# Kernel tuning notes

Measured on AMD Instinct MI355X. Metric: run time of the kernel, lower is better.

Reference implementation:

```python
import jax, jax.numpy as jnp
import numpy as np

N_POINTS = 131072  # 32 clouds * 4096 points
N_SEG = 32


def setup_inputs() -> dict:
    key = jax.random.key(0)
    ks = jax.random.split(key, 8)
    x = jax.random.normal(ks[0], (N_POINTS, 256), dtype=jnp.float32)
    pos = jax.random.normal(ks[1], (N_POINTS, 3), dtype=jnp.float32)
    # sorted segment ids, every segment non-empty (equal-size clouds)
    batch = jnp.repeat(jnp.arange(N_SEG, dtype=jnp.int32), N_POINTS // N_SEG)
    def lin(k, fan_in, fan_out):
        s = 1.0 / np.sqrt(fan_in)
        return jax.random.uniform(k, (fan_in, fan_out), jnp.float32, -s, s)
    W1 = lin(ks[2], 259, 256); b1 = jnp.zeros((256,), jnp.float32)
    W2 = lin(ks[3], 256, 512); b2 = jnp.zeros((512,), jnp.float32)
    W3 = lin(ks[4], 512, 1024); b3 = jnp.zeros((1024,), jnp.float32)
    return {"x": x, "pos": pos, "batch": batch,
            "W1": W1, "b1": b1, "W2": W2, "b2": b2, "W3": W3, "b3": b3}


def reference(x, pos, batch, W1, b1, W2, b2, W3, b3):
    # concat point features with coordinates: [N, 256+3]
    h = jnp.concatenate([x, pos], axis=1)
    # shared point-wise MLP (Linear + ReLU per layer)
    h = jax.nn.relu(h @ W1 + b1)   # [N, 256]
    h = jax.nn.relu(h @ W2 + b2)   # [N, 512]
    h = jax.nn.relu(h @ W3 + b3)   # [N, 1024]
    # global_max_pool: batch-indexed segment max -> [N_SEG, 1024]
    return jax.ops.segment_max(h, batch, num_segments=N_SEG)
```

## Files before the change

### kernel.cpp

```cpp
#include <hip/hip_runtime.h>
#include <stdint.h>

typedef unsigned short ushort_t;
typedef short shortx8 __attribute__((ext_vector_type(8)));
typedef float floatx4 __attribute__((ext_vector_type(4)));
typedef unsigned short ushortx8 __attribute__((ext_vector_type(8)));

__device__ __forceinline__ unsigned short f2bf(float f) {
  union { float f; unsigned int u; } v; v.f = f;
  unsigned int u = v.u;
  return (unsigned short)((u + 0x7fffu + ((u >> 16) & 1u)) >> 16);
}

__device__ __forceinline__ void gload_lds16(const void* g, void* l) {
  __builtin_amdgcn_global_load_lds(
      (const __attribute__((address_space(1))) unsigned int*)g,
      (__attribute__((address_space(3))) unsigned int*)l, 16, 0, 0);
}

__global__ void prep_w_k(const float* __restrict__ W1, const float* __restrict__ W2,
                         const float* __restrict__ W3, ushort_t* __restrict__ W1T,
                         ushort_t* __restrict__ W2T, ushort_t* __restrict__ W3T) {
  int idx = blockIdx.x * blockDim.x + threadIdx.x;
  const float* in; ushort_t* out; int K, N;
  if (idx < 256 * 256)                  { in = W1; out = W1T; K = 256; N = 256; }
  else if (idx < 256 * 256 + 512 * 256) { idx -= 256 * 256; in = W2; out = W2T; K = 256; N = 512; }
  else if (idx < 256 * 256 + 512 * 256 + 1024 * 512) {
    idx -= 256 * 256 + 512 * 256; in = W3; out = W3T; K = 512; N = 1024;
  } else return;
  int n = idx / K, k = idx - n * K;
  out[idx] = f2bf(in[k * N + n]);
}

template <int K, int NOUT, int MODE>
__global__ __launch_bounds__(256, 2) void gemm_kernel(
    const ushort_t* __restrict__ A, const ushort_t* __restrict__ BT,
    const float* __restrict__ bias, ushort_t* __restrict__ C,
    const float* __restrict__ pos, const float* __restrict__ W1tail,
    float* __restrict__ pool, const float* __restrict__ Afp) {
  __shared__ __align__(16) ushort_t As[128 * 64];
  __shared__ __align__(16) ushort_t Bs[128 * 64];

  constexpr int GY = NOUT / 128;
  const int wlin = blockIdx.x + blockIdx.y * gridDim.x;
  const int nwg = gridDim.x * GY;
  const int swz = (wlin & 7) * (nwg >> 3) + (wlin >> 3);
  const int m0 = (swz / GY) * 128;
  const int n0 = (swz % GY) * 128;
  const int tid = threadIdx.x;
  const int w = tid >> 6;
  const int l = tid & 63;
  const int wm = w >> 1, wn = w & 1;
  const int lane16 = l & 15, lq = l >> 4;
  const int s7 = lane16 & 7;

  const int srow = l >> 3;
  const int sg = (l & 7) ^ srow;

  floatx4 acc[4][4] = {};

  for (int k0 = 0; k0 < K; k0 += 64) {
    if (MODE == 1) {
#pragma unroll
      for (int rep = 0; rep < 4; ++rep) {
        const int g = rep * 256 + tid;
        const int row = g >> 3, slot = g & 7;
        const int sgr = slot ^ (row & 7);
        const float4* src = (const float4*)(Afp + (size_t)(m0 + row) * K + k0 + sgr * 8);
        float4 a = src[0], b = src[1];
        ushortx8 v;
        v[0] = f2bf(a.x); v[1] = f2bf(a.y); v[2] = f2bf(a.z); v[3] = f2bf(a.w);
        v[4] = f2bf(b.x); v[5] = f2bf(b.y); v[6] = f2bf(b.z); v[7] = f2bf(b.w);
        *(ushortx8*)(As + row * 64 + slot * 8) = v;
      }
    } else {
#pragma unroll
      for (int r = 0; r < 4; ++r) {
        const int c = r * 4 + w;
        const int row = c * 8 + srow;
        gload_lds16(A + (size_t)(m0 + row) * K + k0 + sg * 8, As + c * 512);
      }
    }
#pragma unroll
    for (int r = 0; r < 4; ++r) {
      const int c = r * 4 + w;
      const int row = c * 8 + srow;
      gload_lds16(BT + (size_t)(n0 + row) * K + k0 + sg * 8, Bs + c * 512);
    }
    __syncthreads();
#pragma unroll
    for (int kk = 0; kk < 2; ++kk) {
      shortx8 af[4], bfr[4];
#pragma unroll
      for (int i = 0; i < 4; ++i) {
        const int row = wm * 64 + i * 16 + lane16;
        af[i] = *(const shortx8*)(As + row * 64 + ((kk * 4 + lq) ^ s7) * 8);
      }
#pragma unroll
      for (int j = 0; j < 4; ++j) {
        const int row = wn * 64 + j * 16 + lane16;
        bfr[j] = *(const shortx8*)(Bs + row * 64 + ((kk * 4 + lq) ^ s7) * 8);
      }
#pragma unroll
      for (int i = 0; i < 4; ++i)
#pragma unroll
        for (int j = 0; j < 4; ++j)
          acc[i][j] = __builtin_amdgcn_mfma_f32_16x16x32_bf16(af[i], bfr[j], acc[i][j], 0, 0, 0);
    }
    __syncthreads();
  }

  float bv[4];
#pragma unroll
  for (int j = 0; j < 4; ++j) bv[j] = bias[n0 + wn * 64 + j * 16 + lane16];

#pragma unroll
  for (int i = 0; i < 4; ++i) {
#pragma unroll
    for (int r = 0; r < 4; ++r) {
      int m = m0 + wm * 64 + i * 16 + lq * 4 + r;
      float p0 = 0.f, p1 = 0.f, p2 = 0.f;
      if (MODE == 1) { p0 = pos[m * 3 + 0]; p1 = pos[m * 3 + 1]; p2 = pos[m * 3 + 2]; }
#pragma unroll
      for (int j = 0; j < 4; ++j) {
        int n = n0 + wn * 64 + j * 16 + lane16;
        float v = acc[i][j][r] + bv[j];
        if (MODE == 1) v += p0 * W1tail[n] + p1 * W1tail[256 + n] + p2 * W1tail[512 + n];
        v = fmaxf(v, 0.0f);
        C[(size_t)m * NOUT + n] = f2bf(v);
      }
    }
  }
}

template <int K, int NOUT, int MODE>
__global__ __launch_bounds__(512, 2) void gemm256_kernel(
    const ushort_t* __restrict__ A, const ushort_t* __restrict__ BT,
    const float* __restrict__ bias, ushort_t* __restrict__ C,
    float* __restrict__ pool) {
  __shared__ __align__(16) ushort_t As[2][256 * 64];
  __shared__ __align__(16) ushort_t Bs[2][256 * 64];

  constexpr int GY = NOUT / 256;
  constexpr int T = K / 64;

  const int wlin = blockIdx.x + blockIdx.y * gridDim.x;
  const int nwg = gridDim.x * GY;
  const int swz = (wlin & 7) * (nwg >> 3) + (wlin >> 3);
  const int m0 = (swz / GY) * 256;
  const int n0 = (swz % GY) * 256;

  const int tid = threadIdx.x;
  const int w8 = tid >> 6;
  const int l = tid & 63;
  const int wm = w8 >> 2, wn = w8 & 3;
  const int lane16 = l & 15, lq = l >> 4;
  const int s7 = lane16 & 7;

  const int sgl = (l & 7) ^ (l >> 3);
  const int lrow = l >> 3;
  const int arow0 = w8 << 3;
  const int brow0 = ((w8 >> 1) << 6) + ((w8 & 1) << 3);

  floatx4 acc[2][4][4] = {};
  shortx8 af[4][2];
  shortx8 bfr[4][2];

#define STAGEA(bb, tt, h, rb)                                                  \
  do {                                                                         \
    const int base_ = (h)*64 + (rb)*128 + arow0;                               \
    gload_lds16(A + (size_t)(m0 + base_ + lrow) * K + (tt)*64 + sgl * 8,       \
                &As[bb][base_ * 64]);                                          \
  } while (0)
#define STAGEB(bb, tt, h, rb)                                                  \
  do {                                                                         \
    const int base_ = brow0 + (h)*32 + (rb)*16;                                \
    gload_lds16(BT + (size_t)(n0 + base_ + lrow) * K + (tt)*64 + sgl * 8,      \
                &Bs[bb][base_ * 64]);                                          \
  } while (0)
#define STAGE_ALL(bb, tt)                                                      \
  do {                                                                         \
    STAGEA(bb, tt, 0, 0); STAGEA(bb, tt, 0, 1);                                \
    STAGEB(bb, tt, 0, 0); STAGEB(bb, tt, 0, 1);                                \
    STAGEB(bb, tt, 1, 0); STAGEB(bb, tt, 1, 1);                                \
    STAGEA(bb, tt, 1, 0); STAGEA(bb, tt, 1, 1);                                \
  } while (0)
#define READA(bb, mh)                                                          \
  {                                                                            \
    _Pragma("unroll") for (int i = 0; i < 4; ++i) {                            \
      const int row_ = wm * 128 + (mh)*64 + i * 16 + lane16;                   \
      _Pragma("unroll") for (int ks = 0; ks < 2; ++ks) {                       \
        const int sl_ = ((ks << 2) | lq) ^ s7;                                 \
        af[i][ks] = *(const shortx8*)(&As[bb][row_ * 64 + sl_ * 8]);           \
      }                                                                        \
    }                                                                          \
  }
#define READB(bb, jh)                                                          \
  {                                                                            \
    _Pragma("unroll") for (int jj = 0; jj < 2; ++jj) {                         \
      const int j_ = (jh)*2 + jj;                                              \
      const int row_ = wn * 64 + j_ * 16 + lane16;                             \
      _Pragma("unroll") for (int ks = 0; ks < 2; ++ks) {                       \
        const int sl_ = ((ks << 2) | lq) ^ s7;                                 \
        bfr[j_][ks] = *(const shortx8*)(&Bs[bb][row_ * 64 + sl_ * 8]);         \
      }                                                                        \
    }                                                                          \
  }
#define DOMFMA(mh, jh)                                                         \
  {                                                                            \
    _Pragma("unroll") for (int ks = 0; ks < 2; ++ks)                           \
    _Pragma("unroll") for (int i = 0; i < 4; ++i)                              \
    _Pragma("unroll") for (int jj = 0; jj < 2; ++jj)                           \
      acc[mh][i][(jh)*2 + jj] = __builtin_amdgcn_mfma_f32_16x16x32_bf16(       \
          af[i][ks], bfr[(jh)*2 + jj][ks], acc[mh][i][(jh)*2 + jj], 0, 0, 0);  \
  }
#define WAITV(n)                                                               \
  do {                                                                         \
    asm volatile("s_waitcnt vmcnt(" #n ")" ::: "memory");                      \
    __builtin_amdgcn_sched_barrier(0);                                         \
  } while (0)
#define BAR()                                                                  \
  do {                                                                         \
    __builtin_amdgcn_sched_barrier(0);                                         \
    asm volatile("" ::: "memory");                                             \
    __builtin_amdgcn_s_barrier();                                              \
    asm volatile("" ::: "memory");                                             \
    __builtin_amdgcn_sched_barrier(0);                                         \
  } while (0)

  STAGE_ALL(0, 0);

  for (int t = 0; t < T; ++t) {
    const int buf = t & 1;
    WAITV(0);
    BAR();
    if (t + 1 < T) STAGE_ALL(buf ^ 1, t + 1);
    READA(buf, 0);
    READB(buf, 0);
    READB(buf, 1);
    __builtin_amdgcn_s_setprio(1);
    DOMFMA(0, 0);
    DOMFMA(0, 1);
    __builtin_amdgcn_s_setprio(0);
    __builtin_amdgcn_sched_barrier(0);
    READA(buf, 1);
    __builtin_amdgcn_s_setprio(1);
    DOMFMA(1, 0);
    DOMFMA(1, 1);
    __builtin_amdgcn_s_setprio(0);
  }
#undef STAGEA
#undef STAGEB
#undef STAGE_ALL
#undef READA
#undef READB
#undef DOMFMA
#undef WAITV
#undef BAR

  float bv[4];
#pragma unroll
  for (int j = 0; j < 4; ++j) bv[j] = bias[n0 + wn * 64 + j * 16 + lane16];

  if (MODE == 2) {
    const int seg = m0 >> 12;
#pragma unroll
    for (int j = 0; j < 4; ++j) {
      float vmax = 0.0f;
#pragma unroll
      for (int mh = 0; mh < 2; ++mh)
#pragma unroll
        for (int i = 0; i < 4; ++i)
#pragma unroll
          for (int r = 0; r < 4; ++r) vmax = fmaxf(vmax, acc[mh][i][j][r] + bv[j]);
      vmax = fmaxf(vmax, 0.0f);
      vmax = fmaxf(vmax, __shfl_xor(vmax, 16, 64));
      vmax = fmaxf(vmax, __shfl_xor(vmax, 32, 64));
      if (l < 16) {
        const int n = n0 + wn * 64 + j * 16 + lane16;
        atomicMax((int*)(pool + (size_t)seg * NOUT + n), __float_as_int(vmax));
      }
    }
  } else {
#pragma unroll
    for (int mh = 0; mh < 2; ++mh)
#pragma unroll
      for (int i = 0; i < 4; ++i)
#pragma unroll
        for (int r = 0; r < 4; ++r) {
          const int m = m0 + wm * 128 + mh * 64 + i * 16 + lq * 4 + r;
#pragma unroll
          for (int j = 0; j < 4; ++j) {
            const int n = n0 + wn * 64 + j * 16 + lane16;
            C[(size_t)m * NOUT + n] = f2bf(fmaxf(acc[mh][i][j][r] + bv[j], 0.0f));
          }
        }
  }
}


extern "C" void kernel_launch(void* const* d_in, const int* in_sizes, int n_in,
                              void* d_out, int out_size, void* d_ws, size_t ws_size,
                              hipStream_t stream) {
  const float* x   = (const float*)d_in[0];
  const float* pos = (const float*)d_in[1];
  const float* W1 = (const float*)d_in[3];
  const float* b1 = (const float*)d_in[4];
  const float* W2 = (const float*)d_in[5];
  const float* b2 = (const float*)d_in[6];
  const float* W3 = (const float*)d_in[7];
  const float* b3 = (const float*)d_in[8];
  float* out = (float*)d_out;

  const int M = in_sizes[0] / 256;

  char* ws = (char*)d_ws;
  ushort_t* H2  = (ushort_t*)ws;
  ushort_t* H1  = (ushort_t*)(ws + (size_t)M * 512 * 2);
  ushort_t* W1T = (ushort_t*)(ws + (size_t)M * 512 * 2 + (size_t)M * 256 * 2);
  ushort_t* W2T = W1T + 256 * 256;
  ushort_t* W3T = W2T + 512 * 256;

  const int ntr = 256 * 256 + 512 * 256 + 1024 * 512;
  prep_w_k<<<(ntr + 255) / 256, 256, 0, stream>>>(W1, W2, W3, W1T, W2T, W3T);

  gemm_kernel<256, 256, 1><<<dim3(M / 128, 2), 256, 0, stream>>>(
      nullptr, W1T, b1, H1, pos, W1 + 256 * 256, nullptr, x);
  gemm256_kernel<256, 512, 0><<<dim3(M / 256, 2), 512, 0, stream>>>(
      H1, W2T, b2, H2, nullptr);
  gemm256_kernel<512, 1024, 2><<<dim3(M / 256, 4), 512, 0, stream>>>(
      H2, W3T, b3, nullptr, out);
}
```

Before: 416.3 us.

## Interleave GEMM global->LDS staging with MFMA phases using fine-grained waits

Splits the per-tile global-to-LDS prefetch into four groups and issues each between LDS fragment reads and MFMA sub-blocks. Partial vmcnt/lgkmcnt waits and extra barriers replace the single full wait plus barrier at the top of each K step, and the last iteration is peeled. The goal is to overlap memory traffic with matrix math and avoid stalling on the whole next tile at once. In exchange it adds more barriers per iteration, and the hand-counted wait values and dropped sched_barriers risk races or compiler reordering.

```diff
diff --git a/kernel.cpp b/kernel.cpp
--- a/kernel.cpp
+++ b/kernel.cpp
@@ -178,13 +178,10 @@
     gload_lds16(BT + (size_t)(n0 + base_ + lrow) * K + (tt)*64 + sgl * 8,      \
                 &Bs[bb][base_ * 64]);                                          \
   } while (0)
-#define STAGE_ALL(bb, tt)                                                      \
-  do {                                                                         \
-    STAGEA(bb, tt, 0, 0); STAGEA(bb, tt, 0, 1);                                \
-    STAGEB(bb, tt, 0, 0); STAGEB(bb, tt, 0, 1);                                \
-    STAGEB(bb, tt, 1, 0); STAGEB(bb, tt, 1, 1);                                \
-    STAGEA(bb, tt, 1, 0); STAGEA(bb, tt, 1, 1);                                \
-  } while (0)
+#define STAGE_GA0(bb, tt) do { STAGEA(bb, tt, 0, 0); STAGEA(bb, tt, 0, 1); } while (0)
+#define STAGE_GB0(bb, tt) do { STAGEB(bb, tt, 0, 0); STAGEB(bb, tt, 0, 1); } while (0)
+#define STAGE_GB1(bb, tt) do { STAGEB(bb, tt, 1, 0); STAGEB(bb, tt, 1, 1); } while (0)
+#define STAGE_GA1(bb, tt) do { STAGEA(bb, tt, 1, 0); STAGEA(bb, tt, 1, 1); } while (0)
 #define READA(bb, mh)                                                          \
   {                                                                            \
     _Pragma("unroll") for (int i = 0; i < 4; ++i) {                            \
@@ -214,49 +211,84 @@
       acc[mh][i][(jh)*2 + jj] = __builtin_amdgcn_mfma_f32_16x16x32_bf16(       \
           af[i][ks], bfr[(jh)*2 + jj][ks], acc[mh][i][(jh)*2 + jj], 0, 0, 0);  \
   }
-#define WAITV(n)                                                               \
-  do {                                                                         \
-    asm volatile("s_waitcnt vmcnt(" #n ")" ::: "memory");                      \
-    __builtin_amdgcn_sched_barrier(0);                                         \
-  } while (0)
-#define BAR()                                                                  \
-  do {                                                                         \
-    __builtin_amdgcn_sched_barrier(0);                                         \
-    asm volatile("" ::: "memory");                                             \
-    __builtin_amdgcn_s_barrier();                                              \
-    asm volatile("" ::: "memory");                                             \
-    __builtin_amdgcn_sched_barrier(0);                                         \
-  } while (0)
-
-  STAGE_ALL(0, 0);
-
-  for (int t = 0; t < T; ++t) {
+#define WAITV(n) asm volatile("s_waitcnt vmcnt(" #n ")" ::: "memory")
+#define WAITL0() asm volatile("s_waitcnt lgkmcnt(0)")
+#define WAITL8() asm volatile("s_waitcnt lgkmcnt(8)")
+#define BAR() __builtin_amdgcn_s_barrier()
+#define PRIO1() __builtin_amdgcn_s_setprio(1)
+#define PRIO0() __builtin_amdgcn_s_setprio(0)
+
+  STAGE_GA0(0, 0); STAGE_GB0(0, 0); STAGE_GB1(0, 0); STAGE_GA1(0, 0);
+  WAITV(4);
+  BAR();
+
+  for (int t = 0; t < T - 1; ++t) {
     const int buf = t & 1;
-    WAITV(0);
-    BAR();
-    if (t + 1 < T) STAGE_ALL(buf ^ 1, t + 1);
+    const int nbuf = buf ^ 1;
     READA(buf, 0);
     READB(buf, 0);
+    STAGE_GA0(nbuf, t + 1);
+    WAITL8();
+    WAITV(4);
+    BAR();
+    WAITL0();
+    PRIO1(); DOMFMA(0, 0); PRIO0();
+    BAR();
     READB(buf, 1);
-    __builtin_amdgcn_s_setprio(1);
-    DOMFMA(0, 0);
-    DOMFMA(0, 1);
-    __builtin_amdgcn_s_setprio(0);
-    __builtin_amdgcn_sched_barrier(0);
+    STAGE_GB0(nbuf, t + 1);
+    WAITV(4);
+    BAR();
+    WAITL0();
+    PRIO1(); DOMFMA(0, 1); PRIO0();
+    BAR();
     READA(buf, 1);
-    __builtin_amdgcn_s_setprio(1);
-    DOMFMA(1, 0);
-    DOMFMA(1, 1);
-    __builtin_amdgcn_s_setprio(0);
+    STAGE_GB1(nbuf, t + 1);
+    BAR();
+    WAITL0();
+    PRIO1(); DOMFMA(1, 0); PRIO0();
+    BAR();
+    STAGE_GA1(nbuf, t + 1);
+    WAITV(4);
+    BAR();
+    PRIO1(); DOMFMA(1, 1); PRIO0();
+    BAR();
+  }
+  {
+    const int buf = (T - 1) & 1;
+    READA(buf, 0);
+    READB(buf, 0);
+    WAITL8();
+    WAITV(2);
+    BAR();
+    WAITL0();
+    PRIO1(); DOMFMA(0, 0); PRIO0();
+    BAR();
+    READB(buf, 1);
+    WAITV(0);
+    BAR();
+    WAITL0();
+    PRIO1(); DOMFMA(0, 1); PRIO0();
+    BAR();
+    READA(buf, 1);
+    BAR();
+    WAITL0();
+    PRIO1(); DOMFMA(1, 0); DOMFMA(1, 1); PRIO0();
   }
 #undef STAGEA
 #undef STAGEB
-#undef STAGE_ALL
+#undef STAGE_GA0
+#undef STAGE_GB0
+#undef STAGE_GB1
+#undef STAGE_GA1
 #undef READA
 #undef READB
 #undef DOMFMA
 #undef WAITV
+#undef WAITL0
+#undef WAITL8
 #undef BAR
+#undef PRIO1
+#undef PRIO0
 
   float bv[4];
 #pragma unroll
```

After: 407.6 us. 1.02x faster.

## Load B operands directly from global in MFMA fragment layout, skip LDS staging

Applied to the files above, without the earlier changes.

The weight matrices for layers 2 and 3 are pre-permuted into an MFMA-fragment-ready blocked layout, so each lane reads its B fragment with one contiguous 16-byte global load instead of staging B through LDS. This halves the shared memory per block and drops the LDS traffic for B. The loop is also restructured so the wait and barrier sit at the end of each iteration. In exchange, every wave reads weights straight from global/L2 with no cross-wave reuse, and the B loads are exposed without double buffering.

```diff
diff --git a/kernel.cpp b/kernel.cpp
--- a/kernel.cpp
+++ b/kernel.cpp
@@ -20,16 +20,22 @@
 
 __global__ void prep_w_k(const float* __restrict__ W1, const float* __restrict__ W2,
                          const float* __restrict__ W3, ushort_t* __restrict__ W1T,
-                         ushort_t* __restrict__ W2T, ushort_t* __restrict__ W3T) {
+                         ushort_t* __restrict__ W2F, ushort_t* __restrict__ W3F) {
   int idx = blockIdx.x * blockDim.x + threadIdx.x;
-  const float* in; ushort_t* out; int K, N;
-  if (idx < 256 * 256)                  { in = W1; out = W1T; K = 256; N = 256; }
-  else if (idx < 256 * 256 + 512 * 256) { idx -= 256 * 256; in = W2; out = W2T; K = 256; N = 512; }
-  else if (idx < 256 * 256 + 512 * 256 + 1024 * 512) {
-    idx -= 256 * 256 + 512 * 256; in = W3; out = W3T; K = 512; N = 1024;
-  } else return;
-  int n = idx / K, k = idx - n * K;
-  out[idx] = f2bf(in[k * N + n]);
+  if (idx < 256 * 256) {
+    int n = idx >> 8, k = idx & 255;
+    W1T[idx] = f2bf(W1[k * 256 + n]);
+  } else if (idx < 256 * 256 + 512 * 256) {
+    int i = idx - 256 * 256;
+    int n = i >> 8, k = i & 255;
+    int dst = ((n >> 4) * 8 + (k >> 5)) * 512 + ((n & 15) + ((k >> 3) & 3) * 16) * 8 + (k & 7);
+    W2F[dst] = f2bf(W2[k * 512 + n]);
+  } else if (idx < 256 * 256 + 512 * 256 + 1024 * 512) {
+    int i = idx - 256 * 256 - 512 * 256;
+    int n = i >> 9, k = i & 511;
+    int dst = ((n >> 4) * 16 + (k >> 5)) * 512 + ((n & 15) + ((k >> 3) & 3) * 16) * 8 + (k & 7);
+    W3F[dst] = f2bf(W3[k * 1024 + n]);
+  }
 }
 
 template <int K, int NOUT, int MODE>
@@ -135,14 +141,14 @@
 
 template <int K, int NOUT, int MODE>
 __global__ __launch_bounds__(512, 2) void gemm256_kernel(
-    const ushort_t* __restrict__ A, const ushort_t* __restrict__ BT,
+    const ushort_t* __restrict__ A, const ushort_t* __restrict__ BF,
     const float* __restrict__ bias, ushort_t* __restrict__ C,
     float* __restrict__ pool) {
   __shared__ __align__(16) ushort_t As[2][256 * 64];
-  __shared__ __align__(16) ushort_t Bs[2][256 * 64];
 
   constexpr int GY = NOUT / 256;
   constexpr int T = K / 64;
+  constexpr int KB = K / 32;
 
   const int wlin = blockIdx.x + blockIdx.y * gridDim.x;
   const int nwg = gridDim.x * GY;
@@ -160,7 +166,7 @@
   const int sgl = (l & 7) ^ (l >> 3);
   const int lrow = l >> 3;
   const int arow0 = w8 << 3;
-  const int brow0 = ((w8 >> 1) << 6) + ((w8 & 1) << 3);
+  const int nbase = (n0 + wn * 64) >> 4;
 
   floatx4 acc[2][4][4] = {};
   shortx8 af[4][2];
@@ -172,17 +178,9 @@
     gload_lds16(A + (size_t)(m0 + base_ + lrow) * K + (tt)*64 + sgl * 8,       \
                 &As[bb][base_ * 64]);                                          \
   } while (0)
-#define STAGEB(bb, tt, h, rb)                                                  \
-  do {                                                                         \
-    const int base_ = brow0 + (h)*32 + (rb)*16;                                \
-    gload_lds16(BT + (size_t)(n0 + base_ + lrow) * K + (tt)*64 + sgl * 8,      \
-                &Bs[bb][base_ * 64]);                                          \
-  } while (0)
-#define STAGE_ALL(bb, tt)                                                      \
+#define STAGE4(bb, tt)                                                         \
   do {                                                                         \
     STAGEA(bb, tt, 0, 0); STAGEA(bb, tt, 0, 1);                                \
-    STAGEB(bb, tt, 0, 0); STAGEB(bb, tt, 0, 1);                                \
-    STAGEB(bb, tt, 1, 0); STAGEB(bb, tt, 1, 1);                                \
     STAGEA(bb, tt, 1, 0); STAGEA(bb, tt, 1, 1);                                \
   } while (0)
 #define READA(bb, mh)                                                          \
@@ -195,15 +193,12 @@
       }                                                                        \
     }                                                                          \
   }
-#define READB(bb, jh)                                                          \
+#define READBG(tt)                                                             \
   {                                                                            \
-    _Pragma("unroll") for (int jj = 0; jj < 2; ++jj) {                         \
-      const int j_ = (jh)*2 + jj;                                              \
-      const int row_ = wn * 64 + j_ * 16 + lane16;                             \
-      _Pragma("unroll") for (int ks = 0; ks < 2; ++ks) {                       \
-        const int sl_ = ((ks << 2) | lq) ^ s7;                                 \
-        bfr[j_][ks] = *(const shortx8*)(&Bs[bb][row_ * 64 + sl_ * 8]);         \
-      }                                                                        \
+    _Pragma("unroll") for (int j = 0; j < 4; ++j)                              \
+    _Pragma("unroll") for (int ks = 0; ks < 2; ++ks) {                         \
+      const int blk_ = (nbase + j) * KB + (tt)*2 + ks;                         \
+      bfr[j][ks] = *(const shortx8*)(BF + (size_t)blk_ * 512 + l * 8);         \
     }                                                                          \
   }
 #define DOMFMA(mh, jh)                                                         \
@@ -214,49 +209,38 @@
       acc[mh][i][(jh)*2 + jj] = __builtin_amdgcn_mfma_f32_16x16x32_bf16(       \
           af[i][ks], bfr[(jh)*2 + jj][ks], acc[mh][i][(jh)*2 + jj], 0, 0, 0);  \
   }
-#define WAITV(n)                                                               \
-  do {                                                                         \
-    asm volatile("s_waitcnt vmcnt(" #n ")" ::: "memory");                      \
-    __builtin_amdgcn_sched_barrier(0);                                         \
-  } while (0)
-#define BAR()                                                                  \
-  do {                                                                         \
-    __builtin_amdgcn_sched_barrier(0);                                         \
-    asm volatile("" ::: "memory");                                             \
-    __builtin_amdgcn_s_barrier();                                              \
-    asm volatile("" ::: "memory");                                             \
-    __builtin_amdgcn_sched_barrier(0);                                         \
-  } while (0)
-
-  STAGE_ALL(0, 0);
+#define WAITV0() asm volatile("s_waitcnt vmcnt(0)" ::: "memory")
+#define CLOB() asm volatile("" ::: "memory")
+#define BARC() asm volatile("s_barrier" ::: "memory")
+#define PRIO1() __builtin_amdgcn_s_setprio(1)
+#define PRIO0() __builtin_amdgcn_s_setprio(0)
+
+  STAGE4(0, 0);
+  WAITV0();
+  BARC();
 
   for (int t = 0; t < T; ++t) {
     const int buf = t & 1;
-    WAITV(0);
-    BAR();
-    if (t + 1 < T) STAGE_ALL(buf ^ 1, t + 1);
+    READBG(t);
+    CLOB();
+    if (t + 1 < T) STAGE4(buf ^ 1, t + 1);
     READA(buf, 0);
-    READB(buf, 0);
-    READB(buf, 1);
-    __builtin_amdgcn_s_setprio(1);
-    DOMFMA(0, 0);
-    DOMFMA(0, 1);
-    __builtin_amdgcn_s_setprio(0);
-    __builtin_amdgcn_sched_barrier(0);
+    PRIO1(); DOMFMA(0, 0); DOMFMA(0, 1); PRIO0();
     READA(buf, 1);
-    __builtin_amdgcn_s_setprio(1);
-    DOMFMA(1, 0);
-    DOMFMA(1, 1);
-    __builtin_amdgcn_s_setprio(0);
+    PRIO1(); DOMFMA(1, 0); DOMFMA(1, 1); PRIO0();
+    WAITV0();
+    BARC();
   }
 #undef STAGEA
-#undef STAGEB
-#undef STAGE_ALL
+#undef STAGE4
 #undef READA
-#undef READB
+#undef READBG
 #undef DOMFMA
-#undef WAITV
-#undef BAR
+#undef WAITV0
+#undef CLOB
+#undef BARC
+#undef PRIO1
+#undef PRIO0
 
   float bv[4];
 #pragma unroll
@@ -318,16 +302,16 @@
   ushort_t* H2  = (ushort_t*)ws;
   ushort_t* H1  = (ushort_t*)(ws + (size_t)M * 512 * 2);
   ushort_t* W1T = (ushort_t*)(ws + (size_t)M * 512 * 2 + (size_t)M * 256 * 2);
-  ushort_t* W2T = W1T + 256 * 256;
-  ushort_t* W3T = W2T + 512 * 256;
+  ushort_t* W2F = W1T + 256 * 256;
+  ushort_t* W3F = W2F + 512 * 256;
 
   const int ntr = 256 * 256 + 512 * 256 + 1024 * 512;
-  prep_w_k<<<(ntr + 255) / 256, 256, 0, stream>>>(W1, W2, W3, W1T, W2T, W3T);
+  prep_w_k<<<(ntr + 255) / 256, 256, 0, stream>>>(W1, W2, W3, W1T, W2F, W3F);
 
   gemm_kernel<256, 256, 1><<<dim3(M / 128, 2), 256, 0, stream>>>(
       nullptr, W1T, b1, H1, pos, W1 + 256 * 256, nullptr, x);
   gemm256_kernel<256, 512, 0><<<dim3(M / 256, 2), 512, 0, stream>>>(
-      H1, W2T, b2, H2, nullptr);
+      H1, W2F, b2, H2, nullptr);
   gemm256_kernel<512, 1024, 2><<<dim3(M / 256, 4), 512, 0, stream>>>(
-      H2, W3T, b3, nullptr, out);
-}
+      H2, W3F, b3, nullptr, out);
+}
```

Result: no change. 421.8 us (+1.3%).
